# Kernel tuning notes

Hardware: AMD Instinct MI355X
Metric: run time of the kernel (lower is better)

## Reference

```python
import jax, jax.numpy as jnp
import numpy as np

N = 100_000   # nodes
E = 3_200_000 # edges (avg degree 32)
K = 10        # propagation hops


def setup_inputs() -> dict:
    key = jax.random.key(0)
    ks = jax.random.split(key, 9)
    x = jax.random.normal(ks[0], (N, 1), dtype=jnp.float32)
    edge_index = jax.random.randint(ks[1], (2, E), 0, N, dtype=jnp.int32)
    # MLP params (lin1: 1->32, lin2: 32->64, fc2: 64->1)
    W1 = jax.random.normal(ks[2], (1, 32), dtype=jnp.float32) * 0.5
    b1 = jnp.zeros((32,), dtype=jnp.float32)
    W2 = jax.random.normal(ks[3], (32, 64), dtype=jnp.float32) * (1.0 / np.sqrt(32))
    b2 = jnp.zeros((64,), dtype=jnp.float32)
    # GPR temp coefficients, Init='Random': uniform(-b, b), b=sqrt(3/(K+1)), L1-normalized
    bound = float(np.sqrt(3.0 / (K + 1)))
    temp = jax.random.uniform(ks[4], (K + 1,), dtype=jnp.float32,
                              minval=-bound, maxval=bound)
    temp = temp / jnp.sum(jnp.abs(temp))
    W_fc = jax.random.normal(ks[5], (64, 1), dtype=jnp.float32) * (1.0 / np.sqrt(64))
    b_fc = jnp.zeros((1,), dtype=jnp.float32)
    return {"x": x, "edge_index": edge_index, "W1": W1, "b1": b1,
            "W2": W2, "b2": b2, "temp": temp, "W_fc": W_fc, "b_fc": b_fc}


def reference(x, edge_index, W1, b1, W2, b2, temp, W_fc, b_fc):
    n = x.shape[0]
    # feature MLP
    h = jax.nn.relu(x @ W1 + b1)       # [N, 32]
    h = jax.nn.relu(h @ W2 + b2)       # [N, 64]
    # gcn_norm with self-loops, edge_weight = 1
    loops = jnp.arange(n, dtype=edge_index.dtype)
    row = jnp.concatenate([edge_index[0], loops])  # source
    col = jnp.concatenate([edge_index[1], loops])  # target (aggregation index)
    ones = jnp.ones(row.shape, dtype=h.dtype)
    deg = jax.ops.segment_sum(ones, col, num_segments=n)
    dinv = jnp.where(deg > 0, jax.lax.rsqrt(deg), 0.0)
    norm = dinv[row] * dinv[col]       # [E+N]
    # K-hop GPR propagation: hidden = sum_k temp[k] * A_hat^k h
    hidden0 = temp[0] * h

    def step(carry, gamma):
        xc, hid = carry
        msg = norm[:, None] * xc[row]                       # gather + scale
        xn = jax.ops.segment_sum(msg, col, num_segments=n)  # scatter-add
        return (xn, hid + gamma * xn), None

    (_, hidden), _ = jax.lax.scan(step, (h, hidden0), temp[1:])
    return hidden @ W_fc + b_fc        # [N, 1]
```

## Files before the change

### kernel.cpp

```cpp
#include <hip/hip_runtime.h>


#define TPB 256
#define BSH 7
#define CAP 5120
#define CH  16384

__global__ void k_zero(int* __restrict__ bcursor, int nb) {
    int i = blockIdx.x * blockDim.x + threadIdx.x;
    if (i < nb) bcursor[i] = 0;
}

__global__ void k_scatter(const int* __restrict__ erow, const int* __restrict__ ecol,
                          int* __restrict__ bcursor, unsigned int* __restrict__ ebuf,
                          int e, int nb) {
    __shared__ int hist[1024];
    __shared__ int base[1024];
    int t = threadIdx.x;
    int s = blockIdx.x * CH;
    int epos = min(e, s + CH);

    for (int b = t; b < nb; b += TPB) hist[b] = 0;
    __syncthreads();
    for (int i = s + t; i < epos; i += TPB)
        atomicAdd(&hist[ecol[i] >> BSH], 1);
    __syncthreads();
    for (int b = t; b < nb; b += TPB) {
        int c = hist[b];
        base[b] = c ? atomicAdd(&bcursor[b], c) : 0;
        hist[b] = 0;
    }
    __syncthreads();
    for (int i = s + t; i < epos; i += TPB) {
        int c = ecol[i];
        int r = erow[i];
        int b = c >> BSH;
        int pos = base[b] + atomicAdd(&hist[b], 1);
        if (pos < CAP)
            ebuf[(size_t)b * CAP + pos] = ((unsigned int)r << BSH) | (unsigned int)(c & (CAP ? ((1 << BSH) - 1) : 0));
    }
}

__global__ void k_bucket(const int* __restrict__ bcursor, unsigned int* __restrict__ ebuf,
                         int* __restrict__ rs, int* __restrict__ re,
                         float* __restrict__ dinv, float* __restrict__ dinv2,
                         float* __restrict__ sdeg, int n) {
    __shared__ unsigned int lbuf[CAP];
    __shared__ int lhist[128];
    __shared__ int lscan[128];
    __shared__ int lcur[128];
    int b = blockIdx.x;
    int t = threadIdx.x;
    int cnt = bcursor[b];
    if (cnt > CAP) cnt = CAP;
    size_t gbase = (size_t)b * CAP;

    if (t < 128) { lhist[t] = 0; }
    __syncthreads();
    for (int j = t; j < cnt; j += TPB) {
        unsigned int p = ebuf[gbase + j];
        lbuf[j] = p;
        atomicAdd(&lhist[p & 127], 1);
    }
    __syncthreads();
    if (t < 128) lscan[t] = lhist[t];
    __syncthreads();
    for (int o = 1; o < 128; o <<= 1) {
        int v = (t < 128 && t >= o) ? lscan[t - o] : 0;
        __syncthreads();
        if (t < 128) lscan[t] += v;
        __syncthreads();
    }
    if (t < 128) {
        int start = lscan[t] - lhist[t];
        lscan[t] = start;
        lcur[t] = 0;
        int node = (b << BSH) + t;
        if (node < n) {
            int deg = lhist[t];
            rs[node] = (int)gbase + start;
            re[node] = (int)gbase + start + deg;
            float d = (float)(deg + 1);
            float di = rsqrtf(d);
            dinv[node] = di;
            dinv2[node] = di * di;
            sdeg[node] = d * di;
        }
    }
    __syncthreads();
    for (int j = t; j < cnt; j += TPB) {
        unsigned int p = lbuf[j];
        int c = p & 127;
        int pos = atomicAdd(&lcur[c], 1);
        ebuf[gbase + lscan[c] + pos] = p >> BSH;
    }
}

__global__ void k_mlp_z(const float* __restrict__ x, const float* __restrict__ W1,
                        const float* __restrict__ b1, const float* __restrict__ W2,
                        const float* __restrict__ b2, const float* __restrict__ Wfc,
                        const float* __restrict__ bfc, const float* __restrict__ temp,
                        const float* __restrict__ dinv,
                        float* __restrict__ u0, float* __restrict__ out, int n) {
    int wid = (blockIdx.x * blockDim.x + threadIdx.x) >> 6;
    int lane = threadIdx.x & 63;
    if (wid >= n) return;
    float xv = x[wid];
    float acc = b2[lane];
#pragma unroll
    for (int j = 0; j < 32; j++) {
        float h1 = fmaxf(fmaf(xv, W1[j], b1[j]), 0.f);
        acc = fmaf(h1, W2[j * 64 + lane], acc);
    }
    float h2 = fmaxf(acc, 0.f);
    float c = h2 * Wfc[lane];
#pragma unroll
    for (int o = 32; o >= 1; o >>= 1) c += __shfl_xor(c, o);
    if (lane == 0) {
        u0[wid] = dinv[wid] * c;
        out[wid] = fmaf(temp[0], c, bfc[0]);
    }
}

__global__ void k_hop(const int* __restrict__ rs, const int* __restrict__ re,
                      const unsigned int* __restrict__ csr_row,
                      const float* __restrict__ dinv2, const float* __restrict__ sdeg,
                      const float* __restrict__ uprev, float* __restrict__ ucur,
                      float* __restrict__ out, const float* __restrict__ temp,
                      int k, int n) {
    int tid = blockIdx.x * blockDim.x + threadIdx.x;
    int node = tid >> 2;
    int sub = tid & 3;
    if (node >= n) return;
    int s = rs[node];
    int epos = re[node];
    float sum = (sub == 0) ? uprev[node] : 0.f;
    for (int i = s + sub; i < epos; i += 4)
        sum += uprev[csr_row[i]];
    sum += __shfl_xor(sum, 1);
    sum += __shfl_xor(sum, 2);
    if (sub == 0) {
        float u = dinv2[node] * sum;
        ucur[node] = u;
        out[node] = fmaf(temp[k] * sdeg[node], u, out[node]);
    }
}

static inline size_t align256(size_t x) { return (x + 255) & ~(size_t)255; }

extern "C" void kernel_launch(void* const* d_in, const int* in_sizes, int n_in,
                              void* d_out, int out_size, void* d_ws, size_t ws_size,
                              hipStream_t stream) {
    const float* x    = (const float*)d_in[0];
    const int*   ei   = (const int*)d_in[1];
    const float* W1   = (const float*)d_in[2];
    const float* b1   = (const float*)d_in[3];
    const float* W2   = (const float*)d_in[4];
    const float* b2   = (const float*)d_in[5];
    const float* temp = (const float*)d_in[6];
    const float* Wfc  = (const float*)d_in[7];
    const float* bfc  = (const float*)d_in[8];

    const int n = in_sizes[0];
    const int e = in_sizes[1] / 2;
    const int K = in_sizes[6] - 1;
    const int nb = (n + 127) >> BSH;

    const int* erow = ei;
    const int* ecol = ei + e;

    float* out = (float*)d_out;

    char* ws = (char*)d_ws;
    int*          bcursor = (int*)ws;          ws += align256((size_t)nb * 4);
    unsigned int* ebuf    = (unsigned int*)ws; ws += align256((size_t)nb * CAP * 4);
    int*          rs      = (int*)ws;          ws += align256((size_t)n * 4);
    int*          re      = (int*)ws;          ws += align256((size_t)n * 4);
    float*        dinv    = (float*)ws;        ws += align256((size_t)n * 4);
    float*        dinv2   = (float*)ws;        ws += align256((size_t)n * 4);
    float*        sdeg    = (float*)ws;        ws += align256((size_t)n * 4);
    float*        u0      = (float*)ws;        ws += align256((size_t)n * 4);
    float*        u1      = (float*)ws;        ws += align256((size_t)n * 4);

    const int gS = (e + CH - 1) / CH;
    const int gW = (n + 3) / 4;
    const int gH = (4 * n + TPB - 1) / TPB;

    k_zero<<<(nb + TPB - 1) / TPB, TPB, 0, stream>>>(bcursor, nb);
    k_scatter<<<gS, TPB, 0, stream>>>(erow, ecol, bcursor, ebuf, e, nb);
    k_bucket<<<nb, TPB, 0, stream>>>(bcursor, ebuf, rs, re, dinv, dinv2, sdeg, n);
    k_mlp_z<<<gW, 256, 0, stream>>>(x, W1, b1, W2, b2, Wfc, bfc, temp, dinv, u0, out, n);

    float* uin = u0;
    float* uout = u1;
    for (int k = 1; k <= K; k++) {
        k_hop<<<gH, TPB, 0, stream>>>(rs, re, ebuf, dinv2, sdeg, uin, uout, out, temp, k, n);
        float* t2 = uin; uin = uout; uout = t2;
    }
}
```

Before: 392.5 us.

## Build compact CSR via coarse 1024-node superbuckets instead of padded 128-node buckets

Switches the edge bucketing from 128-node buckets with fixed padded capacity to 1024-node superbuckets, then a per-superbucket 1024-thread kernel sorts edges by node and writes them into a dense, contiguous CSR with a single row-pointer array. The hop kernel now reads rs[node+1] instead of a separate end array and walks a compact edge list, which should improve locality and cut memory footprint in the ten repeated propagation passes. The cost is a serial prefix over bucket counts by thread 0 in each block and heavier global atomics on fewer bucket cursors in the scatter pass. Capacity overflow beyond CAP1 still silently drops edges.

```diff
diff --git a/kernel.cpp b/kernel.cpp
--- a/kernel.cpp
+++ b/kernel.cpp
@@ -2,97 +2,101 @@
 
 
 #define TPB 256
-#define BSH 7
-#define CAP 5120
-#define CH  16384
-
-__global__ void k_zero(int* __restrict__ bcursor, int nb) {
+#define SBSH 10
+#define CAP1 34304
+#define CH   16384
+
+__global__ void k_zero(int* __restrict__ bcursor, int nsb) {
     int i = blockIdx.x * blockDim.x + threadIdx.x;
-    if (i < nb) bcursor[i] = 0;
+    if (i < nsb) bcursor[i] = 0;
 }
 
 __global__ void k_scatter(const int* __restrict__ erow, const int* __restrict__ ecol,
-                          int* __restrict__ bcursor, unsigned int* __restrict__ ebuf,
-                          int e, int nb) {
-    __shared__ int hist[1024];
-    __shared__ int base[1024];
+                          int* __restrict__ bcursor, unsigned int* __restrict__ ebuf1,
+                          int e, int nsb) {
+    __shared__ int hist[128];
+    __shared__ int base[128];
     int t = threadIdx.x;
     int s = blockIdx.x * CH;
-    int epos = min(e, s + CH);
-
-    for (int b = t; b < nb; b += TPB) hist[b] = 0;
-    __syncthreads();
-    for (int i = s + t; i < epos; i += TPB)
-        atomicAdd(&hist[ecol[i] >> BSH], 1);
-    __syncthreads();
-    for (int b = t; b < nb; b += TPB) {
-        int c = hist[b];
-        base[b] = c ? atomicAdd(&bcursor[b], c) : 0;
-        hist[b] = 0;
-    }
-    __syncthreads();
-    for (int i = s + t; i < epos; i += TPB) {
+    int end = min(e, s + CH);
+
+    if (t < 128) hist[t] = 0;
+    __syncthreads();
+    for (int i = s + t; i < end; i += TPB)
+        atomicAdd(&hist[ecol[i] >> SBSH], 1);
+    __syncthreads();
+    if (t < nsb) {
+        int c = hist[t];
+        base[t] = c ? atomicAdd(&bcursor[t], c) : 0;
+        hist[t] = 0;
+    }
+    __syncthreads();
+    for (int i = s + t; i < end; i += TPB) {
         int c = ecol[i];
         int r = erow[i];
-        int b = c >> BSH;
+        int b = c >> SBSH;
         int pos = base[b] + atomicAdd(&hist[b], 1);
-        if (pos < CAP)
-            ebuf[(size_t)b * CAP + pos] = ((unsigned int)r << BSH) | (unsigned int)(c & (CAP ? ((1 << BSH) - 1) : 0));
-    }
-}
-
-__global__ void k_bucket(const int* __restrict__ bcursor, unsigned int* __restrict__ ebuf,
-                         int* __restrict__ rs, int* __restrict__ re,
-                         float* __restrict__ dinv, float* __restrict__ dinv2,
-                         float* __restrict__ sdeg, int n) {
-    __shared__ unsigned int lbuf[CAP];
-    __shared__ int lhist[128];
-    __shared__ int lscan[128];
-    __shared__ int lcur[128];
+        if (pos < CAP1)
+            ebuf1[(size_t)b * CAP1 + pos] =
+                ((unsigned int)r << SBSH) | (unsigned int)(c & ((1 << SBSH) - 1));
+    }
+}
+
+__global__ void __launch_bounds__(1024)
+k_sub(const int* __restrict__ bcursor, const unsigned int* __restrict__ ebuf1,
+      unsigned int* __restrict__ csr, int* __restrict__ rs,
+      float* __restrict__ dinv, float* __restrict__ dinv2,
+      float* __restrict__ sdeg, int n, int e, int nsb) {
+    __shared__ int hist[1024];
+    __shared__ int hscan[1024];
+    __shared__ int hcur[1024];
+    __shared__ int sbase;
     int b = blockIdx.x;
     int t = threadIdx.x;
-    int cnt = bcursor[b];
-    if (cnt > CAP) cnt = CAP;
-    size_t gbase = (size_t)b * CAP;
-
-    if (t < 128) { lhist[t] = 0; }
-    __syncthreads();
-    for (int j = t; j < cnt; j += TPB) {
-        unsigned int p = ebuf[gbase + j];
-        lbuf[j] = p;
-        atomicAdd(&lhist[p & 127], 1);
-    }
-    __syncthreads();
-    if (t < 128) lscan[t] = lhist[t];
-    __syncthreads();
-    for (int o = 1; o < 128; o <<= 1) {
-        int v = (t < 128 && t >= o) ? lscan[t - o] : 0;
+
+    if (t == 0) {
+        int acc = 0;
+        for (int i = 0; i < b; i++) acc += min(bcursor[i], CAP1);
+        sbase = acc;
+    }
+    hist[t] = 0;
+    __syncthreads();
+
+    int cnt = min(bcursor[b], CAP1);
+    size_t g = (size_t)b * CAP1;
+    for (int j = t; j < cnt; j += 1024)
+        atomicAdd(&hist[ebuf1[g + j] & 1023], 1);
+    __syncthreads();
+
+    hscan[t] = hist[t];
+    __syncthreads();
+    for (int o = 1; o < 1024; o <<= 1) {
+        int v = (t >= o) ? hscan[t - o] : 0;
         __syncthreads();
-        if (t < 128) lscan[t] += v;
+        hscan[t] += v;
         __syncthreads();
     }
-    if (t < 128) {
-        int start = lscan[t] - lhist[t];
-        lscan[t] = start;
-        lcur[t] = 0;
-        int node = (b << BSH) + t;
-        if (node < n) {
-            int deg = lhist[t];
-            rs[node] = (int)gbase + start;
-            re[node] = (int)gbase + start + deg;
-            float d = (float)(deg + 1);
-            float di = rsqrtf(d);
-            dinv[node] = di;
-            dinv2[node] = di * di;
-            sdeg[node] = d * di;
-        }
-    }
-    __syncthreads();
-    for (int j = t; j < cnt; j += TPB) {
-        unsigned int p = lbuf[j];
-        int c = p & 127;
-        int pos = atomicAdd(&lcur[c], 1);
-        ebuf[gbase + lscan[c] + pos] = p >> BSH;
+    int excl = hscan[t] - hist[t];
+    hcur[t] = 0;
+    int node = (b << SBSH) + t;
+    if (node < n) {
+        rs[node] = sbase + excl;
+        float d = (float)(hist[t] + 1);
+        float di = rsqrtf(d);
+        dinv[node] = di;
+        dinv2[node] = di * di;
+        sdeg[node] = d * di;
+    }
+    if (b == 0 && t == 0) rs[n] = e;
+    __syncthreads();
+    hscan[t] = excl;
+    __syncthreads();
+
+    for (int j = t; j < cnt; j += 1024) {
+        unsigned int p = ebuf1[g + j];
+        int sub = p & 1023;
+        int pos = sbase + hscan[sub] + atomicAdd(&hcur[sub], 1);
+        csr[pos] = p >> SBSH;
     }
 }
 
@@ -122,8 +126,7 @@
     }
 }
 
-__global__ void k_hop(const int* __restrict__ rs, const int* __restrict__ re,
-                      const unsigned int* __restrict__ csr_row,
+__global__ void k_hop(const int* __restrict__ rs, const unsigned int* __restrict__ csr,
                       const float* __restrict__ dinv2, const float* __restrict__ sdeg,
                       const float* __restrict__ uprev, float* __restrict__ ucur,
                       float* __restrict__ out, const float* __restrict__ temp,
@@ -133,10 +136,10 @@
     int sub = tid & 3;
     if (node >= n) return;
     int s = rs[node];
-    int epos = re[node];
+    int epos = rs[node + 1];
     float sum = (sub == 0) ? uprev[node] : 0.f;
     for (int i = s + sub; i < epos; i += 4)
-        sum += uprev[csr_row[i]];
+        sum += uprev[csr[i]];
     sum += __shfl_xor(sum, 1);
     sum += __shfl_xor(sum, 2);
     if (sub == 0) {
@@ -164,7 +167,7 @@
     const int n = in_sizes[0];
     const int e = in_sizes[1] / 2;
     const int K = in_sizes[6] - 1;
-    const int nb = (n + 127) >> BSH;
+    const int nsb = (n + (1 << SBSH) - 1) >> SBSH;
 
     const int* erow = ei;
     const int* ecol = ei + e;
@@ -172,10 +175,10 @@
     float* out = (float*)d_out;
 
     char* ws = (char*)d_ws;
-    int*          bcursor = (int*)ws;          ws += align256((size_t)nb * 4);
-    unsigned int* ebuf    = (unsigned int*)ws; ws += align256((size_t)nb * CAP * 4);
-    int*          rs      = (int*)ws;          ws += align256((size_t)n * 4);
-    int*          re      = (int*)ws;          ws += align256((size_t)n * 4);
+    int*          bcursor = (int*)ws;          ws += align256((size_t)128 * 4);
+    unsigned int* ebuf1   = (unsigned int*)ws; ws += align256((size_t)nsb * CAP1 * 4);
+    unsigned int* csr     = (unsigned int*)ws; ws += align256((size_t)e * 4);
+    int*          rs      = (int*)ws;          ws += align256((size_t)(n + 1) * 4);
     float*        dinv    = (float*)ws;        ws += align256((size_t)n * 4);
     float*        dinv2   = (float*)ws;        ws += align256((size_t)n * 4);
     float*        sdeg    = (float*)ws;        ws += align256((size_t)n * 4);
@@ -186,15 +189,15 @@
     const int gW = (n + 3) / 4;
     const int gH = (4 * n + TPB - 1) / TPB;
 
-    k_zero<<<(nb + TPB - 1) / TPB, TPB, 0, stream>>>(bcursor, nb);
-    k_scatter<<<gS, TPB, 0, stream>>>(erow, ecol, bcursor, ebuf, e, nb);
-    k_bucket<<<nb, TPB, 0, stream>>>(bcursor, ebuf, rs, re, dinv, dinv2, sdeg, n);
+    k_zero<<<1, 128, 0, stream>>>(bcursor, nsb);
+    k_scatter<<<gS, TPB, 0, stream>>>(erow, ecol, bcursor, ebuf1, e, nsb);
+    k_sub<<<nsb, 1024, 0, stream>>>(bcursor, ebuf1, csr, rs, dinv, dinv2, sdeg, n, e, nsb);
     k_mlp_z<<<gW, 256, 0, stream>>>(x, W1, b1, W2, b2, Wfc, bfc, temp, dinv, u0, out, n);
 
     float* uin = u0;
     float* uout = u1;
     for (int k = 1; k <= K; k++) {
-        k_hop<<<gH, TPB, 0, stream>>>(rs, re, ebuf, dinv2, sdeg, uin, uout, out, temp, k, n);
+        k_hop<<<gH, TPB, 0, stream>>>(rs, csr, dinv2, sdeg, uin, uout, out, temp, k, n);
         float* t2 = uin; uin = uout; uout = t2;
     }
 }
```

New measurement: 403.3 us. +2.8%, slower.
